# Performance work log

Hardware: AMD Instinct MI355X
Metric: run time of the kernel (lower is better)

## Reference

```python
import jax, jax.numpy as jnp
import numpy as np

# Legacy TF1 tf.image.resize_bilinear semantics (align_corners=False,
# half_pixel_centers=False): src_coord = dst_index * (in_size / out_size).

def _lerp_axis(x, out_size, axis):
    in_size = x.shape[axis]
    scale = in_size / out_size
    coords = jnp.arange(out_size, dtype=jnp.float32) * jnp.float32(scale)
    lo = jnp.floor(coords).astype(jnp.int32)
    hi = jnp.minimum(lo + 1, in_size - 1)
    frac = coords - lo.astype(jnp.float32)
    xlo = jnp.take(x, lo, axis=axis)
    xhi = jnp.take(x, hi, axis=axis)
    bshape = [1] * x.ndim
    bshape[axis] = out_size
    frac = frac.reshape(bshape).astype(x.dtype)
    return xlo + (xhi - xlo) * frac


def _resize_bilinear(img, out_h, out_w):
    # img: (B, H, W, C); separable bilinear, TF1 legacy coordinate mapping
    img = _lerp_axis(img, out_h, axis=1)
    img = _lerp_axis(img, out_w, axis=2)
    return img


def setup_inputs() -> dict:
    key = jax.random.key(0)
    x = jax.random.normal(key, (4, 32, 32, 32, 32), dtype=jnp.float32)
    return {"x": x}


def reference(x) -> jnp.ndarray:
    B, D, H, W, C = x.shape
    R = 64  # out_res
    # (B, D, H, W*C) -> bilinear resize on (D, H) axes
    y = x.reshape(B, D, H, W * C)
    y = _resize_bilinear(y, R, R)  # (B, R, R, W*C)
    # bring W next to a resized axis, resize (W -> R) paired with axis R
    y = y.reshape(B, R, R, W, C)
    y = jnp.transpose(y, (0, 1, 3, 2, 4))      # (B, R, W, R, C)
    y = y.reshape(B, R, W, R * C)
    y = _resize_bilinear(y, R, R)              # (B, R, R, R*C)
    y = y.reshape(B, R, R, R, C)
    y = jnp.transpose(y, (0, 1, 3, 2, 4))      # (B, R, R, R, C)
    return y
```

## Files before the change

kernel.cpp:

```cpp
#include <hip/hip_runtime.h>

typedef float floatx4 __attribute__((ext_vector_type(4)));

__global__ __launch_bounds__(256) void resize3d_up2(
    const floatx4* __restrict__ in, floatx4* __restrict__ out) {
    const int tid = threadIdx.x;
    const int c4 = tid & 7;
    const int w0 = tid >> 3;
    const int bid = blockIdx.x;
    const int h0 = bid & 31;
    const int dg = (bid >> 5) & 15;
    const int b  = bid >> 9;

    const int h1 = min(h0 + 1, 31);
    const int w1 = min(w0 + 1, 31);
    const int d0 = dg << 1;

    const floatx4* inb = in + ((size_t)b << 18) + c4;
#define VIDX(d, h, w) (((d) << 13) + ((h) << 8) + ((w) << 3))
    floatx4 c00 = inb[VIDX(d0, h0, w0)];
    floatx4 c01 = inb[VIDX(d0, h0, w1)];
    floatx4 c10 = inb[VIDX(d0, h1, w0)];
    floatx4 c11 = inb[VIDX(d0, h1, w1)];

    floatx4* outb0 = out + ((size_t)b << 21) + (h0 << 10) + (w0 << 4) + c4;

#define LERP4(a, b) ((a) + ((b) - (a)) * 0.5f)
#define NTST(p, v) __builtin_nontemporal_store((v), (p))
#define EMIT_PLANE(p00, p01, p10, p11, base)                \
    do {                                                    \
        floatx4 eh  = LERP4(p00, p10);       \
        floatx4 eh2 = LERP4(p01, p11);                      \
        NTST((base) + 0,   p00);             \
        NTST((base) + 8,   LERP4(p00, p01)); \
        NTST((base) + 512, eh);                             \
        NTST((base) + 520, LERP4(eh, eh2));  \
    } while (0)

#pragma unroll
    for (int it = 0; it < 2; ++it) {
        const int d  = d0 + it;
        const int dn = min(d + 1, 31);
        floatx4 n00 = inb[VIDX(dn, h0, w0)];
        floatx4 n01 = inb[VIDX(dn, h0, w1)];
        floatx4 n10 = inb[VIDX(dn, h1, w0)];
        floatx4 n11 = inb[VIDX(dn, h1, w1)];

        floatx4 q00 = LERP4(c00, n00);
        floatx4 q01 = LERP4(c01, n01);
        floatx4 q10 = LERP4(c10, n10);
        floatx4 q11 = LERP4(c11, n11);

        floatx4* ob = outb0 + ((size_t)d << 16);
        EMIT_PLANE(c00, c01, c10, c11, ob);
        EMIT_PLANE(q00, q01, q10, q11, ob + 32768);

        c00 = n00; c01 = n01; c10 = n10; c11 = n11;
    }
#undef EMIT_PLANE
#undef NTST
#undef LERP4
#undef VIDX
}

extern "C" void kernel_launch(void* const* d_in, const int* in_sizes, int n_in,
                              void* d_out, int out_size, void* d_ws, size_t ws_size,
                              hipStream_t stream) {
    const floatx4* in = (const floatx4*)d_in[0];
    floatx4* out = (floatx4*)d_out;
    const int grid = out_size / (4 * 16 * 256);
    resize3d_up2<<<grid, 256, 0, stream>>>(in, out);
}
```

Measured before the change: 28.80 us.

## Stage depth-interpolated input slab in LDS and emit fully coalesced output rows

Each block now handles one output depth plane and a band of eight output rows. It first loads five input H-rows (interpolated along depth when the plane is odd) into shared memory, then computes H and W interpolation from LDS. Each thread writes contiguous 16-byte chunks, so whole output rows are stored coalesced instead of as scattered 128-byte fragments. This costs redundant global reads of the overlapping halo row and of depth planes shared by neighbouring output planes, plus a __syncthreads.

```diff
diff --git a/kernel.cpp b/kernel.cpp
--- a/kernel.cpp
+++ b/kernel.cpp
@@ -2,65 +2,57 @@
 
 typedef float floatx4 __attribute__((ext_vector_type(4)));
 
-__global__ __launch_bounds__(256) void resize3d_up2(
+__global__ __launch_bounds__(256) void resize3d_lds(
     const floatx4* __restrict__ in, floatx4* __restrict__ out) {
-    const int tid = threadIdx.x;
-    const int c4 = tid & 7;
-    const int w0 = tid >> 3;
+    __shared__ floatx4 P[5 * 32 * 8];
+
+    const int t = threadIdx.x;
     const int bid = blockIdx.x;
-    const int h0 = bid & 31;
-    const int dg = (bid >> 5) & 15;
+    const int j  = bid & 7;
+    const int od = (bid >> 3) & 63;
     const int b  = bid >> 9;
 
-    const int h1 = min(h0 + 1, 31);
-    const int w1 = min(w0 + 1, 31);
-    const int d0 = dg << 1;
+    const int dlo = od >> 1;
+    const int dhi = min(dlo + 1, 31);
+    const bool dmid = (od & 1) != 0;
 
-    const floatx4* inb = in + ((size_t)b << 18) + c4;
-#define VIDX(d, h, w) (((d) << 13) + ((h) << 8) + ((w) << 3))
-    floatx4 c00 = inb[VIDX(d0, h0, w0)];
-    floatx4 c01 = inb[VIDX(d0, h0, w1)];
-    floatx4 c10 = inb[VIDX(d0, h1, w0)];
-    floatx4 c11 = inb[VIDX(d0, h1, w1)];
+    const floatx4* inb = in + ((size_t)b << 18);
+#pragma unroll
+    for (int r = 0; r < 5; ++r) {
+        const int hg = min(4 * j + r, 31);
+        floatx4 v = inb[(dlo << 13) + (hg << 8) + t];
+        if (dmid) {
+            floatx4 n = inb[(dhi << 13) + (hg << 8) + t];
+            v = v + (n - v) * 0.5f;
+        }
+        P[r * 256 + t] = v;
+    }
+    __syncthreads();
 
-    floatx4* outb0 = out + ((size_t)b << 21) + (h0 << 10) + (w0 << 4) + c4;
-
-#define LERP4(a, b) ((a) + ((b) - (a)) * 0.5f)
-#define NTST(p, v) __builtin_nontemporal_store((v), (p))
-#define EMIT_PLANE(p00, p01, p10, p11, base)                \
-    do {                                                    \
-        floatx4 eh  = LERP4(p00, p10);       \
-        floatx4 eh2 = LERP4(p01, p11);                      \
-        NTST((base) + 0,   p00);             \
-        NTST((base) + 8,   LERP4(p00, p01)); \
-        NTST((base) + 512, eh);                             \
-        NTST((base) + 520, LERP4(eh, eh2));  \
-    } while (0)
+    const int c4  = t & 7;
+    const int wq  = t >> 4;
+    const int fwp = (t >> 3) & 1;
+    floatx4* ob = out + ((size_t)b << 21) + (od << 15) + (j << 12);
 
 #pragma unroll
-    for (int it = 0; it < 2; ++it) {
-        const int d  = d0 + it;
-        const int dn = min(d + 1, 31);
-        floatx4 n00 = inb[VIDX(dn, h0, w0)];
-        floatx4 n01 = inb[VIDX(dn, h0, w1)];
-        floatx4 n10 = inb[VIDX(dn, h1, w0)];
-        floatx4 n11 = inb[VIDX(dn, h1, w1)];
-
-        floatx4 q00 = LERP4(c00, n00);
-        floatx4 q01 = LERP4(c01, n01);
-        floatx4 q10 = LERP4(c10, n10);
-        floatx4 q11 = LERP4(c11, n11);
-
-        floatx4* ob = outb0 + ((size_t)d << 16);
-        EMIT_PLANE(c00, c01, c10, c11, ob);
-        EMIT_PLANE(q00, q01, q10, q11, ob + 32768);
-
-        c00 = n00; c01 = n01; c10 = n10; c11 = n11;
+    for (int kw = 0; kw < 2; ++kw) {
+        const int w0 = kw ? 16 + wq : wq;
+        const int w1 = min(w0 + 1, 31);
+#pragma unroll
+        for (int m = 0; m < 8; ++m) {
+            const int h0 = m >> 1;
+            floatx4 a = P[(h0 * 32 + w0) * 8 + c4];
+            floatx4 bb = P[(h0 * 32 + w1) * 8 + c4];
+            if (m & 1) {
+                floatx4 a1 = P[((h0 + 1) * 32 + w0) * 8 + c4];
+                floatx4 b1 = P[((h0 + 1) * 32 + w1) * 8 + c4];
+                a  = a  + (a1 - a)  * 0.5f;
+                bb = bb + (b1 - bb) * 0.5f;
+            }
+            floatx4 res = fwp ? (a + (bb - a) * 0.5f) : a;
+            __builtin_nontemporal_store(res, ob + (m * 2 + kw) * 256 + t);
+        }
     }
-#undef EMIT_PLANE
-#undef NTST
-#undef LERP4
-#undef VIDX
 }
 
 extern "C" void kernel_launch(void* const* d_in, const int* in_sizes, int n_in,
@@ -68,6 +60,6 @@
                               hipStream_t stream) {
     const floatx4* in = (const floatx4*)d_in[0];
     floatx4* out = (floatx4*)d_out;
-    const int grid = out_size / (4 * 16 * 256);
-    resize3d_up2<<<grid, 256, 0, stream>>>(in, out);
+    const int grid = 4 * 64 * 8;
+    resize3d_lds<<<grid, 256, 0, stream>>>(in, out);
 }
```

Result: slower. 30.18 us (+4.8%).
